# Optimization experiments

Measured on AMD Instinct MI355X. Metric: run time of the kernel, lower is better.

The kernel has to match this reference:

```python
import jax, jax.numpy as jnp
import numpy as np

B, D_IN, H, C, K, ND = 65536, 1024, 512, 2, 4, 7
LN_EPS = 1e-5
CE_W = jnp.array([0.1, 0.9], dtype=jnp.float32)


def setup_inputs() -> dict:
    key = jax.random.key(0)
    ks = jax.random.split(key, 12)
    x = jax.random.normal(ks[0], (B, D_IN), dtype=jnp.float32)
    labels = jax.random.randint(ks[1], (B,), 0, C)
    domain = jax.random.randint(ks[2], (B,), 0, ND)
    fc1_w = jax.random.normal(ks[3], (120, D_IN), dtype=jnp.float32) / np.sqrt(D_IN)
    fc1_b = jnp.zeros((120,), dtype=jnp.float32)
    fc2_w = jax.random.normal(ks[4], (H, 120), dtype=jnp.float32) / np.sqrt(120)
    fc2_b = jnp.zeros((H,), dtype=jnp.float32)
    ln_g = jnp.ones((H,), dtype=jnp.float32)
    ln_b = jnp.zeros((H,), dtype=jnp.float32)
    sms = 0.1 * jax.random.normal(ks[5], (K + 1, H, C), dtype=jnp.float32)
    sm_biases = 0.1 * jax.random.normal(ks[6], (K + 1, C), dtype=jnp.float32)
    embs = 1e-4 * jax.random.normal(ks[7], (ND, K), dtype=jnp.float32)
    cs_wt = jnp.asarray(0.1, dtype=jnp.float32) + 1e-4 * jax.random.normal(ks[8], (), dtype=jnp.float32)
    return {"x": x, "labels": labels, "domain": domain, "fc1_w": fc1_w, "fc1_b": fc1_b,
            "fc2_w": fc2_w, "fc2_b": fc2_b, "ln_g": ln_g, "ln_b": ln_b,
            "sms": sms, "sm_biases": sm_biases, "embs": embs, "cs_wt": cs_wt}


def _weighted_ce(logits, labels, w):
    # torch CrossEntropyLoss(weight=w): sum_i w[y_i]*nll_i / sum_i w[y_i]
    logp = jax.nn.log_softmax(logits, axis=-1)
    nll = -jnp.take_along_axis(logp, labels[:, None], axis=1)[:, 0]
    wl = w[labels]
    return jnp.sum(wl * nll) / jnp.sum(wl)


def reference(x, labels, domain, fc1_w, fc1_b, fc2_w, fc2_b, ln_g, ln_b, sms, sm_biases, embs, cs_wt):
    h = jax.nn.relu(x @ fc1_w.T + fc1_b)           # [B,120]
    h = jax.nn.relu(h @ fc2_w.T + fc2_b)           # [B,H]
    mu = jnp.mean(h, axis=-1, keepdims=True)
    var = jnp.var(h, axis=-1, keepdims=True)
    h = (h - mu) / jnp.sqrt(var + LN_EPS) * ln_g + ln_b

    # common classifier (expert 0)
    logits_common = h @ sms[0] + sm_biases[0]      # [B,C]

    # domain mixture weights
    dom1h = jax.nn.one_hot(domain, ND, dtype=jnp.float32)
    c_wts = dom1h @ embs                           # [B,K]
    c_wts = jnp.tanh(jnp.concatenate([jnp.full((h.shape[0], 1), 1.0, jnp.float32) * cs_wt, c_wts], axis=1))  # [B,K+1]

    # reordered einsum chain: K+1 small GEMMs then weighted sum (avoids [B,K+1,H] weight tensor)
    per_k = jnp.einsum('bh,khc->bkc', h, sms)      # [B,K+1,C]
    logits_spec = jnp.einsum('bk,bkc->bc', c_wts, per_k) + c_wts @ sm_biases  # [B,C]

    specific_loss = _weighted_ce(logits_spec, labels, CE_W)
    class_loss = _weighted_ce(logits_common, labels, CE_W)

    # orthogonality penalty: per-class gram of expert weight columns vs identity
    cps = jnp.einsum('khc,jhc->ckj', sms, sms)     # [C,K+1,K+1]
    orth_loss = jnp.mean((cps - jnp.eye(K + 1, dtype=jnp.float32)[None]) ** 2)

    loss = class_loss + specific_loss + orth_loss
    return (loss, logits_common, class_loss, specific_loss, orth_loss)
```

## Files before the change

### kernel.cpp

```cpp
#include <hip/hip_runtime.h>
#include <hip/hip_bf16.h>

typedef __attribute__((ext_vector_type(8))) short short8;
typedef __attribute__((ext_vector_type(4))) float floatx4;
typedef __attribute__((ext_vector_type(8))) unsigned short ushort8;

#define BTOT 65536
#define WS_W1BF   0u
#define WS_W2BF   262144u
#define WS_GBF    393216u
#define WS_CONST  409600u
#define WS_H1BF   524288u
#define WS_PART   17301504u

__device__ __forceinline__ unsigned short f2bf(float f) {
  unsigned u = __float_as_uint(f);
  unsigned r = u + 0x7FFFu + ((u >> 16) & 1u);
  return (unsigned short)(r >> 16);
}

__device__ __forceinline__ void gload16(const void* g, void* l) {
  __builtin_amdgcn_global_load_lds(
      (const __attribute__((address_space(1))) unsigned int*)g,
      (__attribute__((address_space(3))) unsigned int*)l, 16, 0, 0);
}

__global__ __launch_bounds__(256) void k0_prep(
    const float* __restrict__ w1, const float* __restrict__ w2,
    const float* __restrict__ ln_g, const float* __restrict__ ln_b,
    const float* __restrict__ sms, const float* __restrict__ smb,
    const float* __restrict__ embs, const float* __restrict__ cs,
    unsigned char* __restrict__ ws) {
  const int blk = blockIdx.x, tid = threadIdx.x;
  if (blk < 32) {
    for (int g = blk * 256 + tid; g < 16384; g += 32 * 256) {
      int ks = g >> 10, d = g & 1023;
      int n = d >> 3, cp = d & 7, c = cp ^ (n & 7);
      ushort8 u;
      if (n < 120) {
        const float* s = w1 + n * 1024 + ks * 64 + c * 8;
        float4 v0 = *(const float4*)s, v1 = *(const float4*)(s + 4);
        u[0] = f2bf(v0.x); u[1] = f2bf(v0.y); u[2] = f2bf(v0.z); u[3] = f2bf(v0.w);
        u[4] = f2bf(v1.x); u[5] = f2bf(v1.y); u[6] = f2bf(v1.z); u[7] = f2bf(v1.w);
      } else {
#pragma unroll
        for (int j = 0; j < 8; ++j) u[j] = 0;
      }
      *(ushort8*)(ws + WS_W1BF + (unsigned)g * 16) = u;
    }
  } else if (blk < 40) {
    for (int g = (blk - 32) * 256 + tid; g < 8192; g += 8 * 256) {
      int n = g >> 4, cp = g & 15, c = cp ^ (n & 7);
      ushort8 u;
#pragma unroll
      for (int j = 0; j < 8; ++j) {
        int k = c * 8 + j;
        u[j] = (k < 120) ? f2bf(w2[n * 120 + k]) : (unsigned short)0;
      }
      *(ushort8*)(ws + WS_W2BF + (unsigned)g * 16) = u;
    }
  } else if (blk == 40) {
    for (int e = tid; e < 1024; e += 256) {
      int t = e >> 6, lane = e & 63, q = lane & 15, l4 = lane >> 4;
      ushort8 u;
#pragma unroll
      for (int j = 0; j < 8; ++j) {
        int k = t * 32 + l4 * 8 + j;
        float v = 0.f;
        if (q < 10) { int kk = q >> 1, c = q & 1; v = ln_g[k] * sms[kk * 1024 + k * 2 + c]; }
        u[j] = f2bf(v);
      }
      *(ushort8*)(ws + WS_GBF + (unsigned)e * 16) = u;
    }
  } else {
    float* cst = (float*)(ws + WS_CONST);
    int lane = tid & 63, w = tid >> 6;
    for (int q = w; q < 10; q += 4) {
      int kk = q >> 1, c = q & 1;
      float s = 0.f;
#pragma unroll
      for (int i = 0; i < 8; ++i) { int k = lane + 64 * i; s += ln_b[k] * sms[kk * 1024 + k * 2 + c]; }
#pragma unroll
      for (int o = 32; o >= 1; o >>= 1) s += __shfl_xor(s, o);
      if (lane == 0) cst[q] = s + smb[kk * 2 + c];
    }
    if (tid == 0) cst[16] = tanhf(cs[0]);
    if (tid < 28) cst[32 + tid] = tanhf(embs[tid]);
  }
}

__global__ __launch_bounds__(512) void k1_gemm1(
    const float* __restrict__ x, const unsigned char* __restrict__ w1bf,
    const float* __restrict__ b1, unsigned char* __restrict__ h1bf) {
  __shared__ unsigned char lds[24576];
  unsigned char* Xs = lds;
  unsigned char* Ws = lds + 8192;

  const int tid = threadIdx.x, lane = tid & 63, w = tid >> 6;
  const int l15 = lane & 15, l4 = lane >> 4;
  const long row0 = (long)blockIdx.x * 64;

  const int xr = tid >> 3, xc8 = tid & 7;
  const float* xsrc = x + (row0 + xr) * 1024 + xc8 * 8;
  unsigned char* xdst = Xs + xr * 128 + ((xc8 * 16) ^ ((xr & 7) << 4));
  const unsigned char* wsrc = w1bf + w * 2048 + lane * 16;
  unsigned char* wdst0 = Ws + w * 2048;

  const int col = w * 16 + l15;
  const float bias = (col < 120) ? b1[col] : 0.f;

  floatx4 acc[4];
#pragma unroll
  for (int i = 0; i < 4; ++i) acc[i] = floatx4{0.f, 0.f, 0.f, 0.f};

  float4 v0 = *(const float4*)(xsrc);
  float4 v1 = *(const float4*)(xsrc + 4);

  for (int ks = 0; ks < 16; ++ks) {
    __syncthreads();
    gload16(wsrc + ks * 16384, wdst0);
    gload16(wsrc + ks * 16384 + 1024, wdst0 + 1024);
    ushort8 u;
    u[0] = f2bf(v0.x); u[1] = f2bf(v0.y); u[2] = f2bf(v0.z); u[3] = f2bf(v0.w);
    u[4] = f2bf(v1.x); u[5] = f2bf(v1.y); u[6] = f2bf(v1.z); u[7] = f2bf(v1.w);
    *(ushort8*)xdst = u;
    if (ks < 15) {
      v0 = *(const float4*)(xsrc + (ks + 1) * 64);
      v1 = *(const float4*)(xsrc + (ks + 1) * 64 + 4);
    }
    __syncthreads();
#pragma unroll
    for (int ss = 0; ss < 2; ++ss) {
      short8 a[4];
#pragma unroll
      for (int mt = 0; mt < 4; ++mt) {
        int r = mt * 16 + l15;
        a[mt] = *(const short8*)(Xs + r * 128 + ((ss * 64 + l4 * 16) ^ ((r & 7) << 4)));
      }
      short8 b = *(const short8*)(Ws + col * 128 + ((ss * 64 + l4 * 16) ^ ((col & 7) << 4)));
#pragma unroll
      for (int mt = 0; mt < 4; ++mt)
        acc[mt] = __builtin_amdgcn_mfma_f32_16x16x32_bf16(a[mt], b, acc[mt], 0, 0, 0);
    }
  }
  __syncthreads();
  unsigned char* h1s = lds;
#pragma unroll
  for (int mt = 0; mt < 4; ++mt)
#pragma unroll
    for (int r = 0; r < 4; ++r) {
      int row = mt * 16 + l4 * 4 + r;
      float v = acc[mt][r] + bias;
      v = (col < 120) ? (v > 0.f ? v : 0.f) : 0.f;
      *(unsigned short*)(h1s + row * 256 + ((col * 2) ^ ((row & 7) << 4))) = f2bf(v);
    }
  __syncthreads();
  {
    const unsigned char* s = lds + tid * 32;
    unsigned char* d = h1bf + (long)blockIdx.x * 16384 + tid * 32;
    *(float4*)(d) = *(const float4*)(s);
    *(float4*)(d + 16) = *(const float4*)(s + 16);
  }
}

__global__ __launch_bounds__(512) void k2_fused(
    const unsigned char* __restrict__ h1bf, const unsigned char* __restrict__ w2bf,
    const unsigned char* __restrict__ gbf, const float* __restrict__ cst,
    const float* __restrict__ b2, const int* __restrict__ labels,
    const int* __restrict__ domain, float* __restrict__ out,
    float* __restrict__ partials) {
  extern __shared__ unsigned char lds[];
  unsigned char* h1s = lds;
  unsigned char* W2s = lds + 16384;
  unsigned char* h2s = lds;
  unsigned char* Gs  = lds + 65536;
  float* stats = (float*)(lds + 81920);
  float* musig = (float*)(lds + 87040);
  float* Af    = (float*)(lds + 87552);

  const int tid = threadIdx.x, lane = tid & 63, w = tid >> 6;
  const int l15 = lane & 15, l4 = lane >> 4;
  const long row0 = (long)blockIdx.x * 64;
  const int n0 = w * 64;

  {
    const unsigned char* hs = h1bf + (long)blockIdx.x * 16384 + w * 2048 + lane * 16;
    gload16(hs, h1s + w * 2048);
    gload16(hs + 1024, h1s + w * 2048 + 1024);
    const unsigned char* wsrc = w2bf + w * 16384 + lane * 16;
#pragma unroll
    for (int i = 0; i < 16; ++i)
      gload16(wsrc + i * 1024, W2s + w * 16384 + i * 1024);
  }
  float b2v[4];
#pragma unroll
  for (int nt = 0; nt < 4; ++nt) b2v[nt] = b2[n0 + nt * 16 + l15];
  __syncthreads();

  floatx4 acc[4][4];
#pragma unroll
  for (int i = 0; i < 4; ++i)
#pragma unroll
    for (int j = 0; j < 4; ++j) acc[i][j] = floatx4{0.f, 0.f, 0.f, 0.f};
#pragma unroll
  for (int ks = 0; ks < 4; ++ks) {
    short8 a[4], b[4];
#pragma unroll
    for (int mt = 0; mt < 4; ++mt) {
      int r = mt * 16 + l15;
      a[mt] = *(const short8*)(h1s + r * 256 + ((ks * 64 + l4 * 16) ^ ((r & 7) << 4)));
    }
#pragma unroll
    for (int nt = 0; nt < 4; ++nt) {
      int n = n0 + nt * 16 + l15;
      b[nt] = *(const short8*)(W2s + n * 256 + ((ks * 64 + l4 * 16) ^ ((n & 7) << 4)));
    }
#pragma unroll
    for (int mt = 0; mt < 4; ++mt)
#pragma unroll
      for (int nt = 0; nt < 4; ++nt)
        acc[mt][nt] = __builtin_amdgcn_mfma_f32_16x16x32_bf16(a[mt], b[nt], acc[mt][nt], 0, 0, 0);
  }
  __syncthreads();

  {
    const unsigned char* gs = gbf + w * 2048 + lane * 16;
    gload16(gs, Gs + w * 2048);
    gload16(gs + 1024, Gs + w * 2048 + 1024);
  }
#pragma unroll
  for (int mt = 0; mt < 4; ++mt)
#pragma unroll
    for (int nt = 0; nt < 4; ++nt)
#pragma unroll
      for (int r = 0; r < 4; ++r) {
        float v = acc[mt][nt][r] + b2v[nt];
        acc[mt][nt][r] = v > 0.f ? v : 0.f;
      }
#pragma unroll
  for (int mt = 0; mt < 4; ++mt)
#pragma unroll
    for (int r = 0; r < 4; ++r) {
      float s = 0.f, q2 = 0.f;
#pragma unroll
      for (int nt = 0; nt < 4; ++nt) { float v = acc[mt][nt][r]; s += v; q2 += v * v; }
#pragma unroll
      for (int o = 1; o <= 8; o <<= 1) { s += __shfl_xor(s, o); q2 += __shfl_xor(q2, o); }
      if (l15 == 0) {
        int row = mt * 16 + l4 * 4 + r;
        stats[row * 20 + w * 2] = s;
        stats[row * 20 + w * 2 + 1] = q2;
      }
    }
  __syncthreads();

  if (tid < 64) {
    float S = 0.f, Q = 0.f;
#pragma unroll
    for (int j = 0; j < 8; ++j) { S += stats[tid * 20 + j * 2]; Q += stats[tid * 20 + j * 2 + 1]; }
    float mu = S * (1.f / 512.f);
    float var = Q * (1.f / 512.f) - mu * mu;
    musig[tid * 2] = mu;
    musig[tid * 2 + 1] = rsqrtf(var + 1e-5f);
  }
  __syncthreads();

#pragma unroll
  for (int mt = 0; mt < 4; ++mt)
#pragma unroll
    for (int r = 0; r < 4; ++r) {
      int row = mt * 16 + l4 * 4 + r;
      float mu = musig[row * 2], rs = musig[row * 2 + 1];
#pragma unroll
      for (int nt = 0; nt < 4; ++nt) {
        int colc = n0 + nt * 16 + l15;
        float hn = (acc[mt][nt][r] - mu) * rs;
        *(unsigned short*)(h2s + row * 1024 + ((colc * 2) ^ ((row & 7) << 4))) = f2bf(hn);
      }
    }
  __syncthreads();

  if (w < 4) {
    floatx4 a3 = floatx4{0.f, 0.f, 0.f, 0.f};
    int row = w * 16 + l15;
#pragma unroll
    for (int t = 0; t < 16; ++t) {
      short8 aa = *(const short8*)(h2s + row * 1024 + ((t * 64 + l4 * 16) ^ ((row & 7) << 4)));
      short8 bb = *(const short8*)(Gs + t * 1024 + lane * 16);
      a3 = __builtin_amdgcn_mfma_f32_16x16x32_bf16(aa, bb, a3, 0, 0, 0);
    }
#pragma unroll
    for (int reg = 0; reg < 4; ++reg) {
      int orow = w * 16 + l4 * 4 + reg;
      Af[orow * 20 + l15] = a3[reg];
    }
  }
  __syncthreads();

  if (tid < 64) {
    long grow = row0 + tid;
    float pd[10];
#pragma unroll
    for (int q = 0; q < 10; ++q) pd[q] = Af[tid * 20 + q] + cst[q];
    int lab = labels[grow], dm = domain[grow];
    float cw0 = cst[16];
    float ls0 = cw0 * pd[0], ls1 = cw0 * pd[1];
#pragma unroll
    for (int kk = 1; kk < 5; ++kk) {
      float c = cst[32 + dm * 4 + kk - 1];
      ls0 += c * pd[kk * 2];
      ls1 += c * pd[kk * 2 + 1];
    }
    float lc0 = pd[0], lc1 = pd[1];
    out[1 + grow * 2 + 0] = lc0;
    out[1 + grow * 2 + 1] = lc1;
    float m1 = fmaxf(lc0, lc1);
    float lse1 = m1 + logf(expf(lc0 - m1) + expf(lc1 - m1));
    float nllc = lse1 - (lab ? lc1 : lc0);
    float m2 = fmaxf(ls0, ls1);
    float lse2 = m2 + logf(expf(ls0 - m2) + expf(ls1 - m2));
    float nlls = lse2 - (lab ? ls1 : ls0);
    float wl = lab ? 0.9f : 0.1f;
    float wsum = wl, scom = wl * nllc, sspec = wl * nlls;
#pragma unroll
    for (int o = 32; o >= 1; o >>= 1) {
      wsum += __shfl_xor(wsum, o);
      scom += __shfl_xor(scom, o);
      sspec += __shfl_xor(sspec, o);
    }
    if (tid == 0) {
      partials[(long)blockIdx.x * 4] = wsum;
      partials[(long)blockIdx.x * 4 + 1] = scom;
      partials[(long)blockIdx.x * 4 + 2] = sspec;
    }
  }
}

__global__ __launch_bounds__(256) void k3_finalize(
    const float* __restrict__ partials, const float* __restrict__ sms,
    float* __restrict__ out) {
  __shared__ float wsums[4][3];
  __shared__ float ow[4];
  const int tid = threadIdx.x;
  const int lane = tid & 63, wid = tid >> 6;
  float sw = 0.f, sc = 0.f, ss = 0.f;
  for (int i = tid; i < 1024; i += 256) {
    sw += partials[i * 4];
    sc += partials[i * 4 + 1];
    ss += partials[i * 4 + 2];
  }
#pragma unroll
  for (int o = 32; o >= 1; o >>= 1) {
    sw += __shfl_xor(sw, o);
    sc += __shfl_xor(sc, o);
    ss += __shfl_xor(ss, o);
  }
  if (lane == 0) { wsums[wid][0] = sw; wsums[wid][1] = sc; wsums[wid][2] = ss; }

  float osum = 0.f;
  for (int p = wid; p < 50; p += 4) {
    int c = p / 25, kk = (p / 5) % 5, j = p % 5;
    float acc = 0.f;
#pragma unroll
    for (int hh = 0; hh < 8; ++hh) {
      int h = lane + 64 * hh;
      acc += sms[kk * 1024 + h * 2 + c] * sms[j * 1024 + h * 2 + c];
    }
#pragma unroll
    for (int o = 32; o >= 1; o >>= 1) acc += __shfl_xor(acc, o);
    float d = acc - ((kk == j) ? 1.f : 0.f);
    osum += d * d;
  }
  if (lane == 0) ow[wid] = osum;
  __syncthreads();
  if (tid == 0) {
    float SW = 0.f, SC = 0.f, SS = 0.f, OS = 0.f;
    for (int w = 0; w < 4; ++w) {
      SW += wsums[w][0]; SC += wsums[w][1]; SS += wsums[w][2]; OS += ow[w];
    }
    float orth = OS * (1.f / 50.f);
    float cls = SC / SW;
    float spec = SS / SW;
    out[0] = cls + spec + orth;
    out[131073] = cls;
    out[131074] = spec;
    out[131075] = orth;
  }
}

extern "C" void kernel_launch(void* const* d_in, const int* in_sizes, int n_in,
                              void* d_out, int out_size, void* d_ws, size_t ws_size,
                              hipStream_t stream) {
  const float* x      = (const float*)d_in[0];
  const int* labels   = (const int*)d_in[1];
  const int* domain   = (const int*)d_in[2];
  const float* fc1_w  = (const float*)d_in[3];
  const float* fc1_b  = (const float*)d_in[4];
  const float* fc2_w  = (const float*)d_in[5];
  const float* fc2_b  = (const float*)d_in[6];
  const float* ln_g   = (const float*)d_in[7];
  const float* ln_b   = (const float*)d_in[8];
  const float* sms    = (const float*)d_in[9];
  const float* sm_b   = (const float*)d_in[10];
  const float* embs   = (const float*)d_in[11];
  const float* cs_wt  = (const float*)d_in[12];
  float* out = (float*)d_out;
  unsigned char* ws = (unsigned char*)d_ws;

  (void)hipFuncSetAttribute((const void*)k2_fused,
                            hipFuncAttributeMaxDynamicSharedMemorySize, 147456);

  hipLaunchKernelGGL(k0_prep, dim3(42), dim3(256), 0, stream,
                     fc1_w, fc2_w, ln_g, ln_b, sms, sm_b, embs, cs_wt, ws);
  hipLaunchKernelGGL(k1_gemm1, dim3(BTOT / 64), dim3(512), 0, stream,
                     x, ws + WS_W1BF, fc1_b, ws + WS_H1BF);
  hipLaunchKernelGGL(k2_fused, dim3(BTOT / 64), dim3(512), 147456, stream,
                     ws + WS_H1BF, ws + WS_W2BF, ws + WS_GBF,
                     (const float*)(ws + WS_CONST), fc2_b,
                     labels, domain, out, (float*)(ws + WS_PART));
  hipLaunchKernelGGL(k3_finalize, dim3(1), dim3(256), 0, stream,
                     (const float*)(ws + WS_PART), sms, out);
}
```

Before: 113.4 us.

## Double-buffer GEMM1 LDS tiles and read GEMM2 weights directly in fragment layout

The first GEMM now double-buffers its X and W1 LDS tiles, prefetching the next K-slice with explicit waitcnt and a single barrier per step. This is meant to overlap global loads with MFMA work and remove one sync per iteration. The prep kernel now writes W2 in per-lane MFMA fragment order, so the fused kernel loads B fragments straight from global/L2 and reads the G matrix from global too. That removes about 70KB of LDS staging plus a barrier and permits higher occupancy, but adds repeated L2 reads of the weights. A few small softmax and store tweaks are also included.

```diff
diff --git a/kernel.cpp b/kernel.cpp
--- a/kernel.cpp
+++ b/kernel.cpp
@@ -50,22 +50,24 @@
     }
   } else if (blk < 40) {
     for (int g = (blk - 32) * 256 + tid; g < 8192; g += 8 * 256) {
-      int n = g >> 4, cp = g & 15, c = cp ^ (n & 7);
+      int lane = g & 63, f = g >> 6;
+      int nt = f & 3, ks = (f >> 2) & 3, w = f >> 4;
+      int n = w * 64 + nt * 16 + (lane & 15);
       ushort8 u;
 #pragma unroll
       for (int j = 0; j < 8; ++j) {
-        int k = c * 8 + j;
+        int k = ks * 32 + (lane >> 4) * 8 + j;
         u[j] = (k < 120) ? f2bf(w2[n * 120 + k]) : (unsigned short)0;
       }
       *(ushort8*)(ws + WS_W2BF + (unsigned)g * 16) = u;
     }
   } else if (blk == 40) {
     for (int e = tid; e < 1024; e += 256) {
-      int t = e >> 6, lane = e & 63, q = lane & 15, l4 = lane >> 4;
+      int t = e >> 6, lane = e & 63, q = lane & 15;
       ushort8 u;
 #pragma unroll
       for (int j = 0; j < 8; ++j) {
-        int k = t * 32 + l4 * 8 + j;
+        int k = t * 32 + (lane >> 4) * 8 + j;
         float v = 0.f;
         if (q < 10) { int kk = q >> 1, c = q & 1; v = ln_g[k] * sms[kk * 1024 + k * 2 + c]; }
         u[j] = f2bf(v);
@@ -92,19 +94,16 @@
 __global__ __launch_bounds__(512) void k1_gemm1(
     const float* __restrict__ x, const unsigned char* __restrict__ w1bf,
     const float* __restrict__ b1, unsigned char* __restrict__ h1bf) {
-  __shared__ unsigned char lds[24576];
-  unsigned char* Xs = lds;
-  unsigned char* Ws = lds + 8192;
-
+  __shared__ unsigned char lds[49152];
   const int tid = threadIdx.x, lane = tid & 63, w = tid >> 6;
   const int l15 = lane & 15, l4 = lane >> 4;
   const long row0 = (long)blockIdx.x * 64;
 
   const int xr = tid >> 3, xc8 = tid & 7;
   const float* xsrc = x + (row0 + xr) * 1024 + xc8 * 8;
-  unsigned char* xdst = Xs + xr * 128 + ((xc8 * 16) ^ ((xr & 7) << 4));
+  const unsigned xoff = (unsigned)(xr * 128 + ((xc8 * 16) ^ ((xr & 7) << 4)));
   const unsigned char* wsrc = w1bf + w * 2048 + lane * 16;
-  unsigned char* wdst0 = Ws + w * 2048;
+  const unsigned wdstoff = 16384u + (unsigned)w * 2048;
 
   const int col = w * 16 + l15;
   const float bias = (col < 120) ? b1[col] : 0.f;
@@ -115,35 +114,62 @@
 
   float4 v0 = *(const float4*)(xsrc);
   float4 v1 = *(const float4*)(xsrc + 4);
-
-  for (int ks = 0; ks < 16; ++ks) {
-    __syncthreads();
-    gload16(wsrc + ks * 16384, wdst0);
-    gload16(wsrc + ks * 16384 + 1024, wdst0 + 1024);
+  gload16(wsrc, lds + wdstoff);
+  gload16(wsrc + 1024, lds + wdstoff + 1024);
+  __builtin_amdgcn_sched_barrier(0);
+  {
     ushort8 u;
     u[0] = f2bf(v0.x); u[1] = f2bf(v0.y); u[2] = f2bf(v0.z); u[3] = f2bf(v0.w);
     u[4] = f2bf(v1.x); u[5] = f2bf(v1.y); u[6] = f2bf(v1.z); u[7] = f2bf(v1.w);
-    *(ushort8*)xdst = u;
+    *(ushort8*)(lds + xoff) = u;
+  }
+  v0 = *(const float4*)(xsrc + 64);
+  v1 = *(const float4*)(xsrc + 68);
+  __builtin_amdgcn_sched_barrier(0);
+  asm volatile("s_waitcnt vmcnt(2) lgkmcnt(0)" ::: "memory");
+  __builtin_amdgcn_s_barrier();
+
+  for (int ks = 0; ks < 16; ++ks) {
+    const unsigned cur = ks & 1u, nxt = cur ^ 1u;
     if (ks < 15) {
-      v0 = *(const float4*)(xsrc + (ks + 1) * 64);
-      v1 = *(const float4*)(xsrc + (ks + 1) * 64 + 4);
-    }
-    __syncthreads();
+      gload16(wsrc + (ks + 1) * 16384, lds + 16384 + nxt * 16384 + (wdstoff - 16384));
+      gload16(wsrc + (ks + 1) * 16384 + 1024, lds + 16384 + nxt * 16384 + (wdstoff - 16384) + 1024);
+    }
+    __builtin_amdgcn_sched_barrier(0);
+    if (ks < 15) {
+      ushort8 u;
+      u[0] = f2bf(v0.x); u[1] = f2bf(v0.y); u[2] = f2bf(v0.z); u[3] = f2bf(v0.w);
+      u[4] = f2bf(v1.x); u[5] = f2bf(v1.y); u[6] = f2bf(v1.z); u[7] = f2bf(v1.w);
+      *(ushort8*)(lds + nxt * 8192 + xoff) = u;
+    }
+    if (ks < 14) {
+      v0 = *(const float4*)(xsrc + (ks + 2) * 64);
+      v1 = *(const float4*)(xsrc + (ks + 2) * 64 + 4);
+    }
+    __builtin_amdgcn_sched_barrier(0);
+    const unsigned char* Xc = lds + cur * 8192;
+    const unsigned char* Wc = lds + 16384 + cur * 16384;
 #pragma unroll
     for (int ss = 0; ss < 2; ++ss) {
       short8 a[4];
 #pragma unroll
       for (int mt = 0; mt < 4; ++mt) {
         int r = mt * 16 + l15;
-        a[mt] = *(const short8*)(Xs + r * 128 + ((ss * 64 + l4 * 16) ^ ((r & 7) << 4)));
-      }
-      short8 b = *(const short8*)(Ws + col * 128 + ((ss * 64 + l4 * 16) ^ ((col & 7) << 4)));
+        a[mt] = *(const short8*)(Xc + r * 128 + ((ss * 64 + l4 * 16) ^ ((r & 7) << 4)));
+      }
+      short8 b = *(const short8*)(Wc + col * 128 + ((ss * 64 + l4 * 16) ^ ((col & 7) << 4)));
 #pragma unroll
       for (int mt = 0; mt < 4; ++mt)
         acc[mt] = __builtin_amdgcn_mfma_f32_16x16x32_bf16(a[mt], b, acc[mt], 0, 0, 0);
     }
-  }
-  __syncthreads();
+    if (ks < 14) {
+      asm volatile("s_waitcnt vmcnt(2) lgkmcnt(0)" ::: "memory");
+    } else {
+      asm volatile("s_waitcnt vmcnt(0) lgkmcnt(0)" ::: "memory");
+    }
+    __builtin_amdgcn_s_barrier();
+  }
+
   unsigned char* h1s = lds;
 #pragma unroll
   for (int mt = 0; mt < 4; ++mt)
@@ -163,20 +189,18 @@
   }
 }
 
-__global__ __launch_bounds__(512) void k2_fused(
-    const unsigned char* __restrict__ h1bf, const unsigned char* __restrict__ w2bf,
+__global__ __launch_bounds__(512, 4) void k2_fused(
+    const unsigned char* __restrict__ h1bf, const unsigned char* __restrict__ w2f,
     const unsigned char* __restrict__ gbf, const float* __restrict__ cst,
     const float* __restrict__ b2, const int* __restrict__ labels,
     const int* __restrict__ domain, float* __restrict__ out,
     float* __restrict__ partials) {
   extern __shared__ unsigned char lds[];
   unsigned char* h1s = lds;
-  unsigned char* W2s = lds + 16384;
   unsigned char* h2s = lds;
-  unsigned char* Gs  = lds + 65536;
-  float* stats = (float*)(lds + 81920);
-  float* musig = (float*)(lds + 87040);
-  float* Af    = (float*)(lds + 87552);
+  float* stats = (float*)(lds + 65536);
+  float* musig = (float*)(lds + 70656);
+  float* Af    = (float*)(lds + 71168);
 
   const int tid = threadIdx.x, lane = tid & 63, w = tid >> 6;
   const int l15 = lane & 15, l4 = lane >> 4;
@@ -187,10 +211,6 @@
     const unsigned char* hs = h1bf + (long)blockIdx.x * 16384 + w * 2048 + lane * 16;
     gload16(hs, h1s + w * 2048);
     gload16(hs + 1024, h1s + w * 2048 + 1024);
-    const unsigned char* wsrc = w2bf + w * 16384 + lane * 16;
-#pragma unroll
-    for (int i = 0; i < 16; ++i)
-      gload16(wsrc + i * 1024, W2s + w * 16384 + i * 1024);
   }
   float b2v[4];
 #pragma unroll
@@ -205,29 +225,21 @@
 #pragma unroll
   for (int ks = 0; ks < 4; ++ks) {
     short8 a[4], b[4];
+#pragma unroll
+    for (int nt = 0; nt < 4; ++nt)
+      b[nt] = *(const short8*)(w2f + (((w * 4 + ks) * 4 + nt) * 64 + lane) * 16);
 #pragma unroll
     for (int mt = 0; mt < 4; ++mt) {
       int r = mt * 16 + l15;
       a[mt] = *(const short8*)(h1s + r * 256 + ((ks * 64 + l4 * 16) ^ ((r & 7) << 4)));
     }
 #pragma unroll
-    for (int nt = 0; nt < 4; ++nt) {
-      int n = n0 + nt * 16 + l15;
-      b[nt] = *(const short8*)(W2s + n * 256 + ((ks * 64 + l4 * 16) ^ ((n & 7) << 4)));
-    }
-#pragma unroll
     for (int mt = 0; mt < 4; ++mt)
 #pragma unroll
       for (int nt = 0; nt < 4; ++nt)
         acc[mt][nt] = __builtin_amdgcn_mfma_f32_16x16x32_bf16(a[mt], b[nt], acc[mt][nt], 0, 0, 0);
   }
-  __syncthreads();
-
-  {
-    const unsigned char* gs = gbf + w * 2048 + lane * 16;
-    gload16(gs, Gs + w * 2048);
-    gload16(gs + 1024, Gs + w * 2048 + 1024);
-  }
+
 #pragma unroll
   for (int mt = 0; mt < 4; ++mt)
 #pragma unroll
@@ -286,13 +298,13 @@
 #pragma unroll
     for (int t = 0; t < 16; ++t) {
       short8 aa = *(const short8*)(h2s + row * 1024 + ((t * 64 + l4 * 16) ^ ((row & 7) << 4)));
-      short8 bb = *(const short8*)(Gs + t * 1024 + lane * 16);
+      short8 bb = *(const short8*)(gbf + t * 1024 + lane * 16);
       a3 = __builtin_amdgcn_mfma_f32_16x16x32_bf16(aa, bb, a3, 0, 0, 0);
     }
 #pragma unroll
     for (int reg = 0; reg < 4; ++reg) {
       int orow = w * 16 + l4 * 4 + reg;
-      Af[orow * 20 + l15] = a3[reg];
+      if (l15 < 10) Af[orow * 20 + l15] = a3[reg];
     }
   }
   __syncthreads();
@@ -312,13 +324,12 @@
       ls1 += c * pd[kk * 2 + 1];
     }
     float lc0 = pd[0], lc1 = pd[1];
-    out[1 + grow * 2 + 0] = lc0;
-    out[1 + grow * 2 + 1] = lc1;
-    float m1 = fmaxf(lc0, lc1);
-    float lse1 = m1 + logf(expf(lc0 - m1) + expf(lc1 - m1));
+    *(float2*)(out + 1 + grow * 2) = float2{lc0, lc1};
+    float m1 = fmaxf(lc0, lc1), n1 = fminf(lc0, lc1);
+    float lse1 = m1 + logf(1.f + expf(n1 - m1));
     float nllc = lse1 - (lab ? lc1 : lc0);
-    float m2 = fmaxf(ls0, ls1);
-    float lse2 = m2 + logf(expf(ls0 - m2) + expf(ls1 - m2));
+    float m2 = fmaxf(ls0, ls1), n2 = fminf(ls0, ls1);
+    float lse2 = m2 + logf(1.f + expf(n2 - m2));
     float nlls = lse2 - (lab ? ls1 : ls0);
     float wl = lab ? 0.9f : 0.1f;
     float wsum = wl, scom = wl * nllc, sspec = wl * nlls;
@@ -408,13 +419,13 @@
   unsigned char* ws = (unsigned char*)d_ws;
 
   (void)hipFuncSetAttribute((const void*)k2_fused,
-                            hipFuncAttributeMaxDynamicSharedMemorySize, 147456);
+                            hipFuncAttributeMaxDynamicSharedMemorySize, 76800);
 
   hipLaunchKernelGGL(k0_prep, dim3(42), dim3(256), 0, stream,
                      fc1_w, fc2_w, ln_g, ln_b, sms, sm_b, embs, cs_wt, ws);
   hipLaunchKernelGGL(k1_gemm1, dim3(BTOT / 64), dim3(512), 0, stream,
                      x, ws + WS_W1BF, fc1_b, ws + WS_H1BF);
-  hipLaunchKernelGGL(k2_fused, dim3(BTOT / 64), dim3(512), 147456, stream,
+  hipLaunchKernelGGL(k2_fused, dim3(BTOT / 64), dim3(512), 76800, stream,
                      ws + WS_H1BF, ws + WS_W2BF, ws + WS_GBF,
                      (const float*)(ws + WS_CONST), fc2_b,
                      labels, domain, out, (float*)(ws + WS_PART));
```

After: 109.9 us. 1.03x faster.
